# Performance work log

Measured on AMD Instinct MI355X. Metric: run time of the kernel, lower is better.

## Reference

```python
import jax, jax.numpy as jnp
import numpy as np

N, E, G = 50000, 1000000, 128          # nodes, edges, graphs
NODE_DIM, EDGE_DIM, HID, EMB = 8, 3, 32, 64


def setup_inputs() -> dict:
    key = jax.random.key(0)
    ks = list(jax.random.split(key, 16))
    def nrm(k, shape, s=1.0):
        return jax.random.normal(k, shape, dtype=jnp.float32) * s
    return {
        "x": nrm(ks[0], (N, NODE_DIM)),
        "edge_attr": nrm(ks[1], (E, EDGE_DIM)),
        "the_ratios": jax.random.uniform(ks[2], (5,), dtype=jnp.float32),
        "edge_index": jax.random.randint(ks[3], (2, E), 0, N),
        "batch": jnp.sort(jax.random.randint(ks[4], (N,), 0, G)),
        "the_ids": jax.random.randint(ks[5], (5,), 0, 118),
        # edge_nn: Linear(3,32) -> ReLU -> Linear(32, 8*32)
        "W1": nrm(ks[6], (EDGE_DIM, 32), 0.3), "b1": jnp.zeros((32,), jnp.float32),
        "W2": nrm(ks[7], (32, NODE_DIM * HID), 0.1), "b2": jnp.zeros((NODE_DIM * HID,), jnp.float32),
        "emb": nrm(ks[8], (118, EMB), 0.1),
        # NNConv root weight + bias
        "root": nrm(ks[9], (NODE_DIM, HID), 0.3), "conv_bias": jnp.zeros((HID,), jnp.float32),
        "fc0_w": nrm(ks[10], (HID + EMB, 64), 0.1), "fc0_b": jnp.zeros((64,), jnp.float32),
        "fc1_w": nrm(ks[11], (64, 32), 0.1), "fc1_b": jnp.zeros((32,), jnp.float32),
        "fc2_w": nrm(ks[12], (32, 1), 0.1), "fc2_b": jnp.zeros((1,), jnp.float32),
    }


def reference(x, edge_attr, the_ratios, edge_index, batch, the_ids,
              W1, b1, W2, b2, emb, root, conv_bias,
              fc0_w, fc0_b, fc1_w, fc1_b, fc2_w, fc2_b):
    src, dst = edge_index[0], edge_index[1]
    # per-edge weight matrix from edge MLP: [E, NODE_DIM, HID]
    h = jax.nn.relu(edge_attr @ W1 + b1)
    We = (h @ W2 + b2).reshape(E, NODE_DIM, HID)
    # gather source node feats, per-edge matmul: [E, HID]
    msg = jnp.einsum('ei,eio->eo', x[src], We)
    # scatter-mean to target nodes
    s = jax.ops.segment_sum(msg, dst, num_segments=N)
    cnt = jax.ops.segment_sum(jnp.ones((E,), msg.dtype), dst, num_segments=N)
    agg = s / jnp.maximum(cnt, 1.0)[:, None]
    # NNConv root transform + bias, then ReLU
    h_node = jax.nn.relu(x @ root + agg + conv_bias)
    # global mean pool over graphs
    gs = jax.ops.segment_sum(h_node, batch, num_segments=G)
    gc = jax.ops.segment_sum(jnp.ones((N,), h_node.dtype), batch, num_segments=G)
    pooled = gs / jnp.maximum(gc, 1.0)[:, None]
    # weighted element embedding, broadcast to all graphs
    u = jnp.sum(emb[the_ids] * the_ratios[:, None], axis=0)
    z = jnp.concatenate([pooled, jnp.broadcast_to(u, (G, EMB))], axis=1)
    z = jax.nn.relu(z @ fc0_w + fc0_b)
    z = jax.nn.relu(z @ fc1_w + fc1_b)
    return z @ fc2_w + fc2_b
```

## Files before the change

### kernel.cpp

```cpp
#include <hip/hip_runtime.h>

#define NODE_DIM 8

typedef __attribute__((ext_vector_type(8))) short short8;
typedef __attribute__((ext_vector_type(4))) float f32x4;

#define DOT8(xv, WT) ((xv)[0]*(WT)[0] + (xv)[1]*(WT)[1] + (xv)[2]*(WT)[2] + (xv)[3]*(WT)[3] + \
                      (xv)[4]*(WT)[4] + (xv)[5]*(WT)[5] + (xv)[6]*(WT)[6] + (xv)[7]*(WT)[7])

static __device__ __forceinline__ unsigned pk_bf16(float a, float b) {
    unsigned ua = __float_as_uint(a), ub = __float_as_uint(b);
    ua = (ua + 0x7fffu + ((ua >> 16) & 1u)) >> 16;
    ub = (ub + 0x7fffu + ((ub >> 16) & 1u)) & 0xffff0000u;
    return (ua & 0xffffu) | ub;
}

__global__ __launch_bounds__(256)
void edge_kernel(const float* __restrict__ x,
                 const float* __restrict__ ea,
                 const int* __restrict__ eidx,
                 const float* __restrict__ W1, const float* __restrict__ b1,
                 const float* __restrict__ W2, const float* __restrict__ b2,
                 float* __restrict__ s, int* __restrict__ cnt,
                 int E)
{
    __shared__ __align__(16) short lds_b[18 * 64 * 8];

    const int t = threadIdx.x;

    for (int f = t; f < 18 * 64 * 8; f += 256) {
        const int j   = f & 7;
        const int ln  = (f >> 3) & 63;
        const int fid = f >> 9;
        const int kk  = fid >> 1, ot = fid & 1;
        const int qq  = ln >> 4, ol = ln & 15;
        float v;
        if (kk < 8) v = W2[(kk * 4 + qq) * 256 + j * 32 + ot * 16 + ol];
        else        v = (qq == 0) ? b2[j * 32 + ot * 16 + ol] : 0.f;
        unsigned uv = __float_as_uint(v);
        uv = (uv + 0x7fffu + ((uv >> 16) & 1u)) >> 16;
        lds_b[f] = (short)uv;
    }
    __syncthreads();

    const int lane = t & 63;
    const int e_l  = lane & 15;
    const int q    = lane >> 4;

    float w10[8], w11[8], w12[8], b1r[8];
#pragma unroll
    for (int t2 = 0; t2 < 8; ++t2) {
        const int k = 4 * t2 + q;
        w10[t2] = W1[k]; w11[t2] = W1[32 + k]; w12[t2] = W1[64 + k]; b1r[t2] = b1[k];
    }

    const int wave = blockIdx.x * 4 + (t >> 6);
    const int nwav = gridDim.x * 4;
    const int ngrp = (E + 15) / 16;

    for (int grp = wave; grp < ngrp; grp += nwav) {
        const int base = grp * 16;
        int ej = base + e_l; if (ej >= E) ej = E - 1;
        const int src = eidx[ej];
        const int dst = eidx[E + ej];
        const float ea0 = ea[3 * ej], ea1 = ea[3 * ej + 1], ea2 = ea[3 * ej + 2];
        const float4 xa = *(const float4*)(x + (size_t)(unsigned)src * 8);
        const float4 xb = *(const float4*)(x + (size_t)(unsigned)src * 8 + 4);
        const float xr[8] = {xa.x, xa.y, xa.z, xa.w, xb.x, xb.y, xb.z, xb.w};

        float h[8];
#pragma unroll
        for (int t2 = 0; t2 < 8; ++t2) {
            const float z = b1r[t2] + ea0 * w10[t2] + ea1 * w11[t2] + ea2 * w12[t2];
            h[t2] = z > 0.f ? z : 0.f;
        }

        f32x4 acc0 = {0.f, 0.f, 0.f, 0.f};
        f32x4 acc1 = {0.f, 0.f, 0.f, 0.f};

#pragma unroll
        for (int kk = 0; kk < 9; ++kk) {
            const float hk = (kk < 8) ? h[kk] : 1.f;
            union { short8 v; unsigned u[4]; } af;
#pragma unroll
            for (int p = 0; p < 4; ++p)
                af.u[p] = pk_bf16(hk * xr[2 * p], hk * xr[2 * p + 1]);
            const short8 bf0 = *(const short8*)&lds_b[((kk * 2 + 0) * 64 + lane) * 8];
            const short8 bf1 = *(const short8*)&lds_b[((kk * 2 + 1) * 64 + lane) * 8];
            acc0 = __builtin_amdgcn_mfma_f32_16x16x32_bf16(af.v, bf0, acc0, 0, 0, 0);
            acc1 = __builtin_amdgcn_mfma_f32_16x16x32_bf16(af.v, bf1, acc1, 0, 0, 0);
        }

#pragma unroll
        for (int r = 0; r < 4; ++r) {
            const int m  = q * 4 + r;
            const int eg = base + m;
            const int dr = __shfl(dst, m, 16);
            if (eg < E) {
                atomicAdd(&s[(size_t)(unsigned)dr * 32 + e_l],      acc0[r]);
                atomicAdd(&s[(size_t)(unsigned)dr * 32 + 16 + e_l], acc1[r]);
            }
        }
        if (lane < 16 && base + e_l < E) atomicAdd(&cnt[dst], 1);
    }
}

__global__ __launch_bounds__(256)
void node_pool_kernel(const float* __restrict__ s,
                      const int* __restrict__ cnt,
                      const float* __restrict__ x,
                      const float* __restrict__ root,
                      const float* __restrict__ conv_bias,
                      const int* __restrict__ batch,
                      float* __restrict__ gsum, int N)
{
    __shared__ float red[256];
    const int t    = threadIdx.x;
    const int o    = t & 31;
    const int slot = t >> 5;
    const int base = blockIdx.x * 8;
    const int n    = base + slot;

    float rootr[8];
#pragma unroll
    for (int i = 0; i < 8; ++i) rootr[i] = root[i * 32 + o];
    const float cb = conv_bias[o];

    float v = 0.f;
    int   b = 0;
    if (n < N) {
        b = batch[n];
        const int   c    = cnt[n];
        const float rinv = 1.f / (float)(c > 1 ? c : 1);
        const float* xp  = x + (size_t)n * 8;
        float xv[8];
#pragma unroll
        for (int i = 0; i < 8; ++i) xv[i] = xp[i];
        const float t2 = s[(size_t)n * 32 + o] * rinv + cb + DOT8(xv, rootr);
        v = t2 > 0.f ? t2 : 0.f;
    }

    const int nlast  = (base + 7 < N) ? base + 7 : N - 1;
    const int bfirst = batch[base];
    const int blast  = batch[nlast];

    if (bfirst == blast && base + 7 < N) {
        red[t] = v;
        __syncthreads();
        if (t < 32) {
            float p = 0.f;
#pragma unroll
            for (int c2 = 0; c2 < 8; ++c2) p += red[t + 32 * c2];
            atomicAdd(&gsum[bfirst * 32 + t], p);
        }
    } else {
        if (n < N) atomicAdd(&gsum[b * 32 + o], v);
    }
}

__global__ __launch_bounds__(128)
void mlp_kernel(const float* __restrict__ gsum,
                const int* __restrict__ batch,
                const float* __restrict__ ratios,
                const int* __restrict__ ids,
                const float* __restrict__ emb,
                const float* __restrict__ fc0w, const float* __restrict__ fc0b,
                const float* __restrict__ fc1w, const float* __restrict__ fc1b,
                const float* __restrict__ fc2w, const float* __restrict__ fc2b,
                float* __restrict__ out, int N)
{
    __shared__ float zs[96];
    __shared__ float z1[64];
    __shared__ float z2[32];
    __shared__ int seg[2];

    const int g = blockIdx.x;
    const int t = threadIdx.x;

    if (t < 2) {
        const int target = g + t;
        int lo = 0, hi = N;
        while (lo < hi) {
            const int mid = (lo + hi) >> 1;
            if (batch[mid] < target) lo = mid + 1; else hi = mid;
        }
        seg[t] = lo;
    }
    __syncthreads();

    float c = (float)(seg[1] - seg[0]);
    if (c < 1.f) c = 1.f;

    if (t < 32) zs[t] = gsum[g * 32 + t] / c;
    if (t >= 32 && t < 96) {
        const int j = t - 32;
        float u = 0.f;
#pragma unroll
        for (int r = 0; r < 5; ++r) u += ratios[r] * emb[(size_t)ids[r] * 64 + j];
        zs[32 + j] = u;
    }
    __syncthreads();

    if (t < 64) {
        float a = fc0b[t];
        for (int k = 0; k < 96; ++k) a += zs[k] * fc0w[k * 64 + t];
        z1[t] = a > 0.f ? a : 0.f;
    }
    __syncthreads();

    if (t < 32) {
        float a = fc1b[t];
        for (int k = 0; k < 64; ++k) a += z1[k] * fc1w[k * 32 + t];
        z2[t] = a > 0.f ? a : 0.f;
    }
    __syncthreads();

    if (t == 0) {
        float a = fc2b[0];
        for (int k = 0; k < 32; ++k) a += z2[k] * fc2w[k];
        out[g] = a;
    }
}

extern "C" void kernel_launch(void* const* d_in, const int* in_sizes, int n_in,
                              void* d_out, int out_size, void* d_ws, size_t ws_size,
                              hipStream_t stream)
{
    const float* x         = (const float*)d_in[0];
    const float* ea        = (const float*)d_in[1];
    const float* ratios    = (const float*)d_in[2];
    const int*   eidx      = (const int*)  d_in[3];
    const int*   batch     = (const int*)  d_in[4];
    const int*   ids       = (const int*)  d_in[5];
    const float* W1        = (const float*)d_in[6];
    const float* b1        = (const float*)d_in[7];
    const float* W2        = (const float*)d_in[8];
    const float* b2        = (const float*)d_in[9];
    const float* emb       = (const float*)d_in[10];
    const float* root      = (const float*)d_in[11];
    const float* conv_bias = (const float*)d_in[12];
    const float* fc0w      = (const float*)d_in[13];
    const float* fc0b      = (const float*)d_in[14];
    const float* fc1w      = (const float*)d_in[15];
    const float* fc1b      = (const float*)d_in[16];
    const float* fc2w      = (const float*)d_in[17];
    const float* fc2b      = (const float*)d_in[18];

    const int N = in_sizes[0] / NODE_DIM;
    const int E = in_sizes[1] / 3;
    const int G = out_size;

    float* s    = (float*)d_ws;
    int*   cnt  = (int*)((char*)d_ws + (size_t)N * 32 * 4);
    float* gsum = (float*)((char*)d_ws + (size_t)N * 32 * 4 + (size_t)N * 4);
    (void)hipMemsetAsync(d_ws, 0, (size_t)N * 32 * 4 + (size_t)N * 4 + (size_t)G * 32 * 4, stream);

    edge_kernel<<<2048, 256, 0, stream>>>(x, ea, eidx, W1, b1, W2, b2, s, cnt, E);
    node_pool_kernel<<<(N + 7) / 8, 256, 0, stream>>>(s, cnt, x, root, conv_bias,
                                                      batch, gsum, N);
    mlp_kernel<<<G, 128, 0, stream>>>(gsum, batch, ratios, ids, emb,
                                      fc0w, fc0b, fc1w, fc1b, fc2w, fc2b,
                                      (float*)d_out, N);
}
```

Measured before the change: 280.5 us.

## Replace atomic scatter-mean with CSR sort by destination and segmented gather

Builds a CSR of edges by destination with histogram, single-block scan and atomic scatter kernels, then computes per-edge messages in sorted order into a dense msg buffer. A gather kernel reduces each node's contiguous messages and fuses root transform, ReLU and graph pooling. This removes the float atomics on node sums, but adds three preprocessing launches, a serial 1024-thread scan, and a 128 MB message write and read-back. The old atomic path is kept as a fallback when the workspace is too small.

```diff
diff --git a/kernel.cpp b/kernel.cpp
--- a/kernel.cpp
+++ b/kernel.cpp
@@ -16,16 +16,209 @@
 }
 
 __global__ __launch_bounds__(256)
-void edge_kernel(const float* __restrict__ x,
-                 const float* __restrict__ ea,
-                 const int* __restrict__ eidx,
-                 const float* __restrict__ W1, const float* __restrict__ b1,
-                 const float* __restrict__ W2, const float* __restrict__ b2,
-                 float* __restrict__ s, int* __restrict__ cnt,
-                 int E)
+void hist_kernel(const int* __restrict__ eidx, int* __restrict__ cnt, int E)
+{
+    const int e = blockIdx.x * blockDim.x + threadIdx.x;
+    if (e < E) atomicAdd(&cnt[eidx[E + e]], 1);
+}
+
+__global__ __launch_bounds__(1024)
+void scan_kernel(const int* __restrict__ cnt, int* __restrict__ rowptr,
+                 int* __restrict__ next, int N, int E)
+{
+    __shared__ int part[1024];
+    const int t  = threadIdx.x;
+    const int CH = (N + 1023) >> 10;
+    const int lo = t * CH;
+    const int hi = (lo + CH < N) ? lo + CH : N;
+
+    int sum = 0;
+    for (int i = lo; i < hi; ++i) sum += cnt[i];
+    part[t] = sum;
+    __syncthreads();
+
+    for (int off = 1; off < 1024; off <<= 1) {
+        const int v = (t >= off) ? part[t - off] : 0;
+        __syncthreads();
+        part[t] += v;
+        __syncthreads();
+    }
+
+    int run = (t == 0) ? 0 : part[t - 1];
+    for (int i = lo; i < hi; ++i) {
+        rowptr[i] = run;
+        next[i]   = run;
+        run += cnt[i];
+    }
+    if (t == 1023) rowptr[N] = E;
+}
+
+__global__ __launch_bounds__(256)
+void scatter_kernel(const int* __restrict__ eidx, int* __restrict__ next,
+                    int* __restrict__ perm, int E)
+{
+    const int e = blockIdx.x * blockDim.x + threadIdx.x;
+    if (e < E) {
+        const int pos = atomicAdd(&next[eidx[E + e]], 1);
+        perm[pos] = e;
+    }
+}
+
+__global__ __launch_bounds__(256)
+void edge_kernel_csr(const float* __restrict__ x,
+                     const float* __restrict__ ea,
+                     const int* __restrict__ eidx,
+                     const int* __restrict__ perm,
+                     const float* __restrict__ W1, const float* __restrict__ b1,
+                     const float* __restrict__ W2, const float* __restrict__ b2,
+                     float* __restrict__ msg, int E)
 {
     __shared__ __align__(16) short lds_b[18 * 64 * 8];
-
+    const int t = threadIdx.x;
+
+    for (int f = t; f < 18 * 64 * 8; f += 256) {
+        const int j   = f & 7;
+        const int ln  = (f >> 3) & 63;
+        const int fid = f >> 9;
+        const int kk  = fid >> 1, ot = fid & 1;
+        const int qq  = ln >> 4, ol = ln & 15;
+        float v;
+        if (kk < 8) v = W2[(kk * 4 + qq) * 256 + j * 32 + ot * 16 + ol];
+        else        v = (qq == 0) ? b2[j * 32 + ot * 16 + ol] : 0.f;
+        unsigned uv = __float_as_uint(v);
+        uv = (uv + 0x7fffu + ((uv >> 16) & 1u)) >> 16;
+        lds_b[f] = (short)uv;
+    }
+    __syncthreads();
+
+    const int lane = t & 63;
+    const int e_l  = lane & 15;
+    const int q    = lane >> 4;
+
+    float w10[8], w11[8], w12[8], b1r[8];
+#pragma unroll
+    for (int t2 = 0; t2 < 8; ++t2) {
+        const int k = 4 * t2 + q;
+        w10[t2] = W1[k]; w11[t2] = W1[32 + k]; w12[t2] = W1[64 + k]; b1r[t2] = b1[k];
+    }
+
+    const int wave = blockIdx.x * 4 + (t >> 6);
+    const int nwav = gridDim.x * 4;
+    const int ngrp = (E + 15) / 16;
+
+    for (int grp = wave; grp < ngrp; grp += nwav) {
+        const int base = grp * 16;
+        int slot = base + e_l; if (slot >= E) slot = E - 1;
+        const int ej  = perm[slot];
+        const int src = eidx[ej];
+        const float ea0 = ea[3 * ej], ea1 = ea[3 * ej + 1], ea2 = ea[3 * ej + 2];
+        const float4 xa = *(const float4*)(x + (size_t)(unsigned)src * 8);
+        const float4 xb = *(const float4*)(x + (size_t)(unsigned)src * 8 + 4);
+        const float xr[8] = {xa.x, xa.y, xa.z, xa.w, xb.x, xb.y, xb.z, xb.w};
+
+        float h[8];
+#pragma unroll
+        for (int t2 = 0; t2 < 8; ++t2) {
+            const float z = b1r[t2] + ea0 * w10[t2] + ea1 * w11[t2] + ea2 * w12[t2];
+            h[t2] = z > 0.f ? z : 0.f;
+        }
+
+        f32x4 acc0 = {0.f, 0.f, 0.f, 0.f};
+        f32x4 acc1 = {0.f, 0.f, 0.f, 0.f};
+
+#pragma unroll
+        for (int kk = 0; kk < 9; ++kk) {
+            const float hk = (kk < 8) ? h[kk] : 1.f;
+            union { short8 v; unsigned u[4]; } af;
+#pragma unroll
+            for (int p = 0; p < 4; ++p)
+                af.u[p] = pk_bf16(hk * xr[2 * p], hk * xr[2 * p + 1]);
+            const short8 bf0 = *(const short8*)&lds_b[((kk * 2 + 0) * 64 + lane) * 8];
+            const short8 bf1 = *(const short8*)&lds_b[((kk * 2 + 1) * 64 + lane) * 8];
+            acc0 = __builtin_amdgcn_mfma_f32_16x16x32_bf16(af.v, bf0, acc0, 0, 0, 0);
+            acc1 = __builtin_amdgcn_mfma_f32_16x16x32_bf16(af.v, bf1, acc1, 0, 0, 0);
+        }
+
+#pragma unroll
+        for (int r = 0; r < 4; ++r) {
+            const int row = base + q * 4 + r;
+            if (row < E) {
+                msg[(size_t)row * 32 + e_l]      = acc0[r];
+                msg[(size_t)row * 32 + 16 + e_l] = acc1[r];
+            }
+        }
+    }
+}
+
+__global__ __launch_bounds__(256)
+void gather_pool_kernel(const float* __restrict__ msg,
+                        const int* __restrict__ rowptr,
+                        const float* __restrict__ x,
+                        const float* __restrict__ root,
+                        const float* __restrict__ conv_bias,
+                        const int* __restrict__ batch,
+                        float* __restrict__ gsum, int N)
+{
+    __shared__ float red[256];
+    const int t    = threadIdx.x;
+    const int o    = t & 31;
+    const int slot = t >> 5;
+    const int base = blockIdx.x * 8;
+    const int n    = base + slot;
+
+    float rootr[8];
+#pragma unroll
+    for (int i = 0; i < 8; ++i) rootr[i] = root[i * 32 + o];
+    const float cb = conv_bias[o];
+
+    float v = 0.f;
+    int   b = 0;
+    if (n < N) {
+        b = batch[n];
+        const int startp = rowptr[n], endp = rowptr[n + 1];
+        float sum = 0.f;
+        int i = startp;
+        for (; i + 1 < endp; i += 2)
+            sum += msg[(size_t)i * 32 + o] + msg[(size_t)(i + 1) * 32 + o];
+        if (i < endp) sum += msg[(size_t)i * 32 + o];
+        const int   c    = endp - startp;
+        const float rinv = 1.f / (float)(c > 1 ? c : 1);
+        const float* xp  = x + (size_t)n * 8;
+        float xv[8];
+#pragma unroll
+        for (int k = 0; k < 8; ++k) xv[k] = xp[k];
+        const float t2 = sum * rinv + cb + DOT8(xv, rootr);
+        v = t2 > 0.f ? t2 : 0.f;
+    }
+
+    const int nlast  = (base + 7 < N) ? base + 7 : N - 1;
+    const int bfirst = batch[base];
+    const int blast  = batch[nlast];
+
+    if (bfirst == blast && base + 7 < N) {
+        red[t] = v;
+        __syncthreads();
+        if (t < 32) {
+            float p = 0.f;
+#pragma unroll
+            for (int c2 = 0; c2 < 8; ++c2) p += red[t + 32 * c2];
+            atomicAdd(&gsum[bfirst * 32 + t], p);
+        }
+    } else {
+        if (n < N) atomicAdd(&gsum[b * 32 + o], v);
+    }
+}
+
+__global__ __launch_bounds__(256)
+void edge_kernel_atomic(const float* __restrict__ x,
+                        const float* __restrict__ ea,
+                        const int* __restrict__ eidx,
+                        const float* __restrict__ W1, const float* __restrict__ b1,
+                        const float* __restrict__ W2, const float* __restrict__ b2,
+                        float* __restrict__ s, int* __restrict__ cnt,
+                        int E)
+{
+    __shared__ __align__(16) short lds_b[18 * 64 * 8];
     const int t = threadIdx.x;
 
     for (int f = t; f < 18 * 64 * 8; f += 256) {
@@ -250,15 +443,38 @@
     const int E = in_sizes[1] / 3;
     const int G = out_size;
 
-    float* s    = (float*)d_ws;
-    int*   cnt  = (int*)((char*)d_ws + (size_t)N * 32 * 4);
-    float* gsum = (float*)((char*)d_ws + (size_t)N * 32 * 4 + (size_t)N * 4);
-    (void)hipMemsetAsync(d_ws, 0, (size_t)N * 32 * 4 + (size_t)N * 4 + (size_t)G * 32 * 4, stream);
-
-    edge_kernel<<<2048, 256, 0, stream>>>(x, ea, eidx, W1, b1, W2, b2, s, cnt, E);
-    node_pool_kernel<<<(N + 7) / 8, 256, 0, stream>>>(s, cnt, x, root, conv_bias,
-                                                      batch, gsum, N);
-    mlp_kernel<<<G, 128, 0, stream>>>(gsum, batch, ratios, ids, emb,
-                                      fc0w, fc0b, fc1w, fc1b, fc2w, fc2b,
-                                      (float*)d_out, N);
-}
+    char* p = (char*)d_ws;
+    float* msg    = (float*)p;                      p += (size_t)E * 32 * 4;
+    int*   perm   = (int*)p;                        p += (size_t)E * 4;
+    int*   rowptr = (int*)p;                        p += (size_t)(N + 1) * 4;
+    int*   nxt    = (int*)p;                        p += (size_t)N * 4;
+    int*   cnt    = (int*)p;                        p += (size_t)N * 4;
+    float* gsum   = (float*)p;                      p += (size_t)G * 32 * 4;
+    const size_t need_csr = (size_t)(p - (char*)d_ws);
+
+    if (ws_size >= need_csr) {
+        (void)hipMemsetAsync(cnt, 0, (size_t)N * 4 + (size_t)G * 32 * 4, stream);
+        hist_kernel<<<(E + 255) / 256, 256, 0, stream>>>(eidx, cnt, E);
+        scan_kernel<<<1, 1024, 0, stream>>>(cnt, rowptr, nxt, N, E);
+        scatter_kernel<<<(E + 255) / 256, 256, 0, stream>>>(eidx, nxt, perm, E);
+        edge_kernel_csr<<<2048, 256, 0, stream>>>(x, ea, eidx, perm,
+                                                  W1, b1, W2, b2, msg, E);
+        gather_pool_kernel<<<(N + 7) / 8, 256, 0, stream>>>(msg, rowptr, x, root,
+                                                            conv_bias, batch, gsum, N);
+        mlp_kernel<<<G, 128, 0, stream>>>(gsum, batch, ratios, ids, emb,
+                                          fc0w, fc0b, fc1w, fc1b, fc2w, fc2b,
+                                          (float*)d_out, N);
+    } else {
+        float* s2    = (float*)d_ws;
+        int*   cnt2  = (int*)((char*)d_ws + (size_t)N * 32 * 4);
+        float* gsum2 = (float*)((char*)d_ws + (size_t)N * 32 * 4 + (size_t)N * 4);
+        (void)hipMemsetAsync(d_ws, 0, (size_t)N * 32 * 4 + (size_t)N * 4 + (size_t)G * 32 * 4, stream);
+        edge_kernel_atomic<<<2048, 256, 0, stream>>>(x, ea, eidx, W1, b1, W2, b2,
+                                                     s2, cnt2, E);
+        node_pool_kernel<<<(N + 7) / 8, 256, 0, stream>>>(s2, cnt2, x, root, conv_bias,
+                                                          batch, gsum2, N);
+        mlp_kernel<<<G, 128, 0, stream>>>(gsum2, batch, ratios, ids, emb,
+                                          fc0w, fc0b, fc1w, fc1b, fc2w, fc2b,
+                                          (float*)d_out, N);
+    }
+}
```

After: 453.8 us. 1.62x slower.

## Replace atomic scatter-mean with CSR sort by destination and segmented gather

Applied to the files above, without the earlier changes.

Builds a destination-sorted CSR (histogram, three-pass scan, atomic scatter into a permutation). The edge kernel now processes edges in sorted order and writes per-edge messages to a dense E×32 buffer. A gather kernel then sums each node's segment without float atomics. This removes about 32M float atomics, but adds about 128MB of message writes and reads plus several extra launches. NB ≤ 256 is assumed by scan2.

```diff
diff --git a/kernel.cpp b/kernel.cpp
--- a/kernel.cpp
+++ b/kernel.cpp
@@ -16,16 +16,87 @@
 }
 
 __global__ __launch_bounds__(256)
-void edge_kernel(const float* __restrict__ x,
-                 const float* __restrict__ ea,
-                 const int* __restrict__ eidx,
-                 const float* __restrict__ W1, const float* __restrict__ b1,
-                 const float* __restrict__ W2, const float* __restrict__ b2,
-                 float* __restrict__ s, int* __restrict__ cnt,
-                 int E)
+void hist_kernel(const int* __restrict__ eidx, int* __restrict__ cnt, int E)
+{
+    const int e = blockIdx.x * blockDim.x + threadIdx.x;
+    if (e < E) atomicAdd(&cnt[eidx[E + e]], 1);
+}
+
+__global__ __launch_bounds__(256)
+void scan1_kernel(const int* __restrict__ cnt, int* __restrict__ rowptr,
+                  int* __restrict__ bsum, int N)
+{
+    __shared__ int sh[256];
+    const int t = threadIdx.x;
+    const int i = blockIdx.x * 256 + t;
+    const int v = (i < N) ? cnt[i] : 0;
+    sh[t] = v;
+    __syncthreads();
+#pragma unroll
+    for (int off = 1; off < 256; off <<= 1) {
+        int add = 0;
+        if (t >= off) add = sh[t - off];
+        __syncthreads();
+        if (t >= off) sh[t] += add;
+        __syncthreads();
+    }
+    if (i < N) rowptr[i] = sh[t] - v;
+    if (t == 255) bsum[blockIdx.x] = sh[255];
+}
+
+__global__ __launch_bounds__(256)
+void scan2_kernel(const int* __restrict__ bsum, int* __restrict__ boff, int NB)
+{
+    __shared__ int sh[256];
+    const int t = threadIdx.x;
+    const int v = (t < NB) ? bsum[t] : 0;
+    sh[t] = v;
+    __syncthreads();
+#pragma unroll
+    for (int off = 1; off < 256; off <<= 1) {
+        int add = 0;
+        if (t >= off) add = sh[t - off];
+        __syncthreads();
+        if (t >= off) sh[t] += add;
+        __syncthreads();
+    }
+    if (t < NB) boff[t] = sh[t] - v;
+}
+
+__global__ __launch_bounds__(256)
+void scan3_kernel(int* __restrict__ rowptr, int* __restrict__ nxt,
+                  const int* __restrict__ boff, int N, int E)
+{
+    const int i = blockIdx.x * 256 + threadIdx.x;
+    if (i < N) {
+        const int r = rowptr[i] + boff[i >> 8];
+        rowptr[i] = r;
+        nxt[i]    = r;
+    }
+    if (i == 0) rowptr[N] = E;
+}
+
+__global__ __launch_bounds__(256)
+void scatter_kernel(const int* __restrict__ eidx, int* __restrict__ nxt,
+                    int* __restrict__ perm, int E)
+{
+    const int e = blockIdx.x * blockDim.x + threadIdx.x;
+    if (e < E) {
+        const int pos = atomicAdd(&nxt[eidx[E + e]], 1);
+        perm[pos] = e;
+    }
+}
+
+__global__ __launch_bounds__(256)
+void edge_kernel_csr(const float* __restrict__ x,
+                     const float* __restrict__ ea,
+                     const int* __restrict__ eidx,
+                     const int* __restrict__ perm,
+                     const float* __restrict__ W1, const float* __restrict__ b1,
+                     const float* __restrict__ W2, const float* __restrict__ b2,
+                     float* __restrict__ msg, int E)
 {
     __shared__ __align__(16) short lds_b[18 * 64 * 8];
-
     const int t = threadIdx.x;
 
     for (int f = t; f < 18 * 64 * 8; f += 256) {
@@ -60,9 +131,9 @@
 
     for (int grp = wave; grp < ngrp; grp += nwav) {
         const int base = grp * 16;
-        int ej = base + e_l; if (ej >= E) ej = E - 1;
+        int slot = base + e_l; if (slot >= E) slot = E - 1;
+        const int ej  = perm[slot];
         const int src = eidx[ej];
-        const int dst = eidx[E + ej];
         const float ea0 = ea[3 * ej], ea1 = ea[3 * ej + 1], ea2 = ea[3 * ej + 2];
         const float4 xa = *(const float4*)(x + (size_t)(unsigned)src * 8);
         const float4 xb = *(const float4*)(x + (size_t)(unsigned)src * 8 + 4);
@@ -93,26 +164,23 @@
 
 #pragma unroll
         for (int r = 0; r < 4; ++r) {
-            const int m  = q * 4 + r;
-            const int eg = base + m;
-            const int dr = __shfl(dst, m, 16);
-            if (eg < E) {
-                atomicAdd(&s[(size_t)(unsigned)dr * 32 + e_l],      acc0[r]);
-                atomicAdd(&s[(size_t)(unsigned)dr * 32 + 16 + e_l], acc1[r]);
+            const int row = base + q * 4 + r;
+            if (row < E) {
+                msg[(size_t)row * 32 + e_l]      = acc0[r];
+                msg[(size_t)row * 32 + 16 + e_l] = acc1[r];
             }
         }
-        if (lane < 16 && base + e_l < E) atomicAdd(&cnt[dst], 1);
-    }
-}
-
-__global__ __launch_bounds__(256)
-void node_pool_kernel(const float* __restrict__ s,
-                      const int* __restrict__ cnt,
-                      const float* __restrict__ x,
-                      const float* __restrict__ root,
-                      const float* __restrict__ conv_bias,
-                      const int* __restrict__ batch,
-                      float* __restrict__ gsum, int N)
+    }
+}
+
+__global__ __launch_bounds__(256)
+void gather_pool_kernel(const float* __restrict__ msg,
+                        const int* __restrict__ rowptr,
+                        const float* __restrict__ x,
+                        const float* __restrict__ root,
+                        const float* __restrict__ conv_bias,
+                        const int* __restrict__ batch,
+                        float* __restrict__ gsum, int N)
 {
     __shared__ float red[256];
     const int t    = threadIdx.x;
@@ -130,13 +198,19 @@
     int   b = 0;
     if (n < N) {
         b = batch[n];
-        const int   c    = cnt[n];
+        const int startp = rowptr[n], endp = rowptr[n + 1];
+        float sum = 0.f;
+        int i = startp;
+        for (; i + 1 < endp; i += 2)
+            sum += msg[(size_t)i * 32 + o] + msg[(size_t)(i + 1) * 32 + o];
+        if (i < endp) sum += msg[(size_t)i * 32 + o];
+        const int   c    = endp - startp;
         const float rinv = 1.f / (float)(c > 1 ? c : 1);
         const float* xp  = x + (size_t)n * 8;
         float xv[8];
 #pragma unroll
-        for (int i = 0; i < 8; ++i) xv[i] = xp[i];
-        const float t2 = s[(size_t)n * 32 + o] * rinv + cb + DOT8(xv, rootr);
+        for (int k = 0; k < 8; ++k) xv[k] = xp[k];
+        const float t2 = sum * rinv + cb + DOT8(xv, rootr);
         v = t2 > 0.f ? t2 : 0.f;
     }
 
@@ -249,15 +323,29 @@
     const int N = in_sizes[0] / NODE_DIM;
     const int E = in_sizes[1] / 3;
     const int G = out_size;
-
-    float* s    = (float*)d_ws;
-    int*   cnt  = (int*)((char*)d_ws + (size_t)N * 32 * 4);
-    float* gsum = (float*)((char*)d_ws + (size_t)N * 32 * 4 + (size_t)N * 4);
-    (void)hipMemsetAsync(d_ws, 0, (size_t)N * 32 * 4 + (size_t)N * 4 + (size_t)G * 32 * 4, stream);
-
-    edge_kernel<<<2048, 256, 0, stream>>>(x, ea, eidx, W1, b1, W2, b2, s, cnt, E);
-    node_pool_kernel<<<(N + 7) / 8, 256, 0, stream>>>(s, cnt, x, root, conv_bias,
-                                                      batch, gsum, N);
+    const int NB = (N + 255) / 256;
+
+    char* p = (char*)d_ws;
+    float* msg    = (float*)p;  p += (size_t)E * 32 * 4;
+    int*   perm   = (int*)p;    p += (size_t)E * 4;
+    int*   rowptr = (int*)p;    p += (size_t)(N + 1) * 4;
+    int*   nxt    = (int*)p;    p += (size_t)N * 4;
+    int*   cnt    = (int*)p;    p += (size_t)N * 4;
+    float* gsum   = (float*)p;  p += (size_t)G * 32 * 4;
+    int*   bsum   = (int*)p;    p += 256 * 4;
+    int*   boff   = (int*)p;    p += 256 * 4;
+
+    (void)hipMemsetAsync(cnt, 0, (size_t)N * 4 + (size_t)G * 32 * 4, stream);
+
+    hist_kernel   <<<(E + 255) / 256, 256, 0, stream>>>(eidx, cnt, E);
+    scan1_kernel  <<<NB, 256, 0, stream>>>(cnt, rowptr, bsum, N);
+    scan2_kernel  <<<1, 256, 0, stream>>>(bsum, boff, NB);
+    scan3_kernel  <<<NB, 256, 0, stream>>>(rowptr, nxt, boff, N, E);
+    scatter_kernel<<<(E + 255) / 256, 256, 0, stream>>>(eidx, nxt, perm, E);
+    edge_kernel_csr<<<2048, 256, 0, stream>>>(x, ea, eidx, perm,
+                                              W1, b1, W2, b2, msg, E);
+    gather_pool_kernel<<<(N + 7) / 8, 256, 0, stream>>>(msg, rowptr, x, root,
+                                                        conv_bias, batch, gsum, N);
     mlp_kernel<<<G, 128, 0, stream>>>(gsum, batch, ratios, ids, emb,
                                       fc0w, fc0b, fc1w, fc1b, fc2w, fc2b,
                                       (float*)d_out, N);
```

New measurement: 358.9 us. 1.28x slower.
